# Performance work log

Measured on AMD Instinct MI355X. Metric: run time of the kernel, lower is better.

Reference implementation:

```python
import jax, jax.numpy as jnp
import numpy as np

B, T, C = 2, 2048, 2048
N_HEAD, N_KV_HEAD = 16, 4
HEAD_DIM = C // N_HEAD  # 128
N_REP = N_HEAD // N_KV_HEAD  # 4


def setup_inputs() -> dict:
    key = jax.random.key(0)
    ks = jax.random.split(key, 5)
    x = jax.random.normal(ks[0], (B, T, C), dtype=jnp.float32)
    # RoPE freqs (theta=10000), real cos/sin form of torch's complex freqs_cis
    inv_freq = 1.0 / (10000.0 ** (jnp.arange(0, HEAD_DIM, 2, dtype=jnp.float32) / HEAD_DIM))
    angles = jnp.arange(T, dtype=jnp.float32)[:, None] * inv_freq[None, :]  # [T, HEAD_DIM//2]
    freqs_cos = jnp.cos(angles)
    freqs_sin = jnp.sin(angles)
    s = 0.02
    wq = jax.random.normal(ks[1], (C, C), dtype=jnp.float32) * s
    wk = jax.random.normal(ks[2], (N_KV_HEAD * HEAD_DIM, C), dtype=jnp.float32) * s
    wv = jax.random.normal(ks[3], (N_KV_HEAD * HEAD_DIM, C), dtype=jnp.float32) * s
    wo = jax.random.normal(ks[4], (C, C), dtype=jnp.float32) * s
    return {"x": x, "freqs_cos": freqs_cos, "freqs_sin": freqs_sin,
            "wq": wq, "wk": wk, "wv": wv, "wo": wo}


def _apply_rotary(t, cos, sin):
    # t: [B, T, H, D]; pairs (even, odd) treated as complex, multiplied by cos+i*sin
    tr = t.reshape(*t.shape[:-1], -1, 2)  # [B,T,H,D/2,2]
    t0, t1 = tr[..., 0], tr[..., 1]
    c = cos[None, :, None, :]  # [1,T,1,D/2]
    s = sin[None, :, None, :]
    out = jnp.stack([t0 * c - t1 * s, t0 * s + t1 * c], axis=-1)
    return out.reshape(t.shape)


def reference(x, freqs_cos, freqs_sin, wq, wk, wv, wo):
    b, t, _ = x.shape
    xq = (x @ wq.T).reshape(b, t, N_HEAD, HEAD_DIM)
    xk = (x @ wk.T).reshape(b, t, N_KV_HEAD, HEAD_DIM)
    xv = (x @ wv.T).reshape(b, t, N_KV_HEAD, HEAD_DIM)
    xq = _apply_rotary(xq, freqs_cos, freqs_sin)
    xk = _apply_rotary(xk, freqs_cos, freqs_sin)
    # GQA: repeat_interleave kv heads to n_head
    xk_r = jnp.repeat(xk, N_REP, axis=2)
    xv_r = jnp.repeat(xv, N_REP, axis=2)
    # [B,H,T,D]
    q = xq.transpose(0, 2, 1, 3)
    k = xk_r.transpose(0, 2, 1, 3)
    v = xv_r.transpose(0, 2, 1, 3)
    scale = 1.0 / jnp.sqrt(jnp.float32(HEAD_DIM))
    scores = jnp.einsum('bhtd,bhsd->bhts', q, k) * scale
    causal = jnp.tril(jnp.ones((t, t), dtype=bool))
    scores = jnp.where(causal[None, None], scores, jnp.finfo(scores.dtype).min)
    attn = jax.nn.softmax(scores, axis=-1)
    y = jnp.einsum('bhts,bhsd->bhtd', attn, v)
    y = y.transpose(0, 2, 1, 3).reshape(b, t, C)
    return y @ wo.T
```

## Files before the change

kernel.cpp:

```cpp
#include <hip/hip_runtime.h>

typedef __attribute__((ext_vector_type(8))) __bf16 bf16x8;
typedef __attribute__((ext_vector_type(4))) __bf16 bf16x4;
typedef __attribute__((ext_vector_type(4))) float floatx4;

#define MFMA16x16x32 __builtin_amdgcn_mfma_f32_16x16x32_bf16

__device__ __forceinline__ void async_load16(const void* g, void* l) {
  __builtin_amdgcn_global_load_lds((const __attribute__((address_space(1))) void*)g,
                                   (__attribute__((address_space(3))) void*)l, 16, 0, 0);
}

__global__ __launch_bounds__(256) void cast_all_kernel(const float* __restrict__ x,
                                                       const float* __restrict__ wq,
                                                       const float* __restrict__ wk,
                                                       const float* __restrict__ wv,
                                                       const float* __restrict__ wo,
                                                       __bf16* __restrict__ dst) {
  int i = blockIdx.x * blockDim.x + threadIdx.x;
  const float* src;
  int off;
  if (i < 2097152)      { src = x;  off = 0; }
  else if (i < 3145728) { src = wq; off = 2097152; }
  else if (i < 3407872) { src = wk; off = 3145728; }
  else if (i < 3670016) { src = wv; off = 3407872; }
  else                  { src = wo; off = 3670016; }
  float4 v = ((const float4*)src)[i - off];
  bf16x4 o;
  o[0] = (__bf16)v.x; o[1] = (__bf16)v.y; o[2] = (__bf16)v.z; o[3] = (__bf16)v.w;
  *(bf16x4*)(dst + (size_t)i * 4) = o;
}

template <int MODE>
__global__ __launch_bounds__(256, 3) void gemm_bt(const __bf16* __restrict__ A,
                                                  const __bf16* __restrict__ Bw,
                                                  float* __restrict__ C,
                                                  const float* __restrict__ cs,
                                                  const float* __restrict__ sn,
                                                  __bf16* __restrict__ qb,
                                                  __bf16* __restrict__ kb,
                                                  __bf16* __restrict__ vtg,
                                                  int M, int N, int K) {
  __shared__ __bf16 As[128][64];
  __shared__ __bf16 Bs[128][64];
  const int tid = threadIdx.x;
  const int wave = tid >> 6, lane = tid & 63;
  const int quad = lane >> 4, l16 = lane & 15;
  const int wm = (wave >> 1) * 64, wn = (wave & 1) * 64;
  const int row0 = blockIdx.y * 128, col0 = blockIdx.x * 128;
  const int lr = lane >> 3, ls = lane & 7;
  const int segg = ls ^ lr;
  floatx4 acc[4][4] = {};
  const __bf16* Ab = A + (size_t)row0 * K + segg * 8;
  const __bf16* Bb = Bw + (size_t)col0 * K + segg * 8;
  for (int k0 = 0; k0 < K; k0 += 64) {
    __syncthreads();
#pragma unroll
    for (int i = 0; i < 4; i++) {
      int c = wave * 4 + i;
      int r = c * 8 + lr;
      async_load16(Ab + (size_t)r * K + k0, &As[c * 8][0]);
      async_load16(Bb + (size_t)r * K + k0, &Bs[c * 8][0]);
    }
    __syncthreads();
#pragma unroll
    for (int kk = 0; kk < 64; kk += 32) {
      bf16x8 af[4], bfr[4];
#pragma unroll
      for (int mt = 0; mt < 4; mt++) {
        int row = wm + mt * 16 + l16;
        int seg = ((kk >> 3) + quad) ^ (row & 7);
        af[mt] = *(const bf16x8*)&As[row][seg * 8];
      }
#pragma unroll
      for (int nt = 0; nt < 4; nt++) {
        int row = wn + nt * 16 + l16;
        int seg = ((kk >> 3) + quad) ^ (row & 7);
        bfr[nt] = *(const bf16x8*)&Bs[row][seg * 8];
      }
#pragma unroll
      for (int mt = 0; mt < 4; mt++)
#pragma unroll
        for (int nt = 0; nt < 4; nt++)
          acc[mt][nt] = MFMA16x16x32(af[mt], bfr[nt], acc[mt][nt], 0, 0, 0);
    }
  }
  if (MODE == 0) {
#pragma unroll
    for (int mt = 0; mt < 4; mt++)
#pragma unroll
      for (int nt = 0; nt < 4; nt++)
#pragma unroll
        for (int r = 0; r < 4; r++) {
          int row = row0 + wm + mt * 16 + quad * 4 + r;
          int col = col0 + wn + nt * 16 + l16;
          C[(size_t)row * N + col] = acc[mt][nt][r];
        }
  } else {
#pragma unroll
    for (int mt = 0; mt < 4; mt++)
#pragma unroll
      for (int nt = 0; nt < 4; nt++) {
        const int cbase = col0 + wn + nt * 16;
        const int c = cbase + l16;
#pragma unroll
        for (int r = 0; r < 4; r++) {
          int row = row0 + wm + mt * 16 + quad * 4 + r;
          int t = row & 2047;
          float v = acc[mt][nt][r];
          float vp = __shfl_xor(v, 1);
          if (cbase < 2048) {
            int i = (c & 127) >> 1;
            float co = cs[t * 64 + i], si = sn[t * 64 + i];
            qb[(size_t)row * 2048 + c] = (__bf16)(v * co + ((c & 1) ? vp : -vp) * si);
          } else if (cbase < 2560) {
            int i = (c & 127) >> 1;
            float co = cs[t * 64 + i], si = sn[t * 64 + i];
            kb[(size_t)row * 512 + c - 2048] = (__bf16)(v * co + ((c & 1) ? vp : -vp) * si);
          } else {
            int vd = c - 2560;
            vtg[((size_t)(row >> 11) * 512 + vd) * 2048 + t] = (__bf16)v;
          }
        }
      }
  }
}

__global__ __launch_bounds__(256, 2) void attn_kernel(const __bf16* __restrict__ qb,
                                                      const __bf16* __restrict__ kb,
                                                      const __bf16* __restrict__ vtg,
                                                      __bf16* __restrict__ yb) {
  const int id = blockIdx.x;
  const int q1 = id >> 8;
  const int cc = id & 255;
  const int kvh = cc & 3;
  const int b = (cc >> 2) & 1;
  const int s5 = (cc >> 3) & 31;
  const int tile = q1 ? (63 - s5) : s5;
  const int tid = threadIdx.x, wave = tid >> 6, lane = tid & 63;
  const int h = kvh * 4 + wave;
  const int quad = lane >> 4, l16 = lane & 15;
  const int q0 = tile * 32;
  __shared__ __bf16 Ks[2][64][128];
  __shared__ __bf16 Vt[2][128][64];
  __shared__ __bf16 Ps[4][2][16][64];
  const __bf16* kbase = kb + (size_t)b * 2048 * 512 + kvh * 128;
  const __bf16* vbase = vtg + ((size_t)b * 512 + kvh * 128) * 2048;
  const float cexp = 0.1275411391f;
  const int klr4 = lane >> 4, kls = lane & 15;
  const int vlr8 = lane >> 3, vls = lane & 7;

  auto stage = [&](int pb, int s0) {
#pragma unroll
    for (int i = 0; i < 4; i++) {
      int ch = wave * 4 + i;
      int row = ch * 4 + klr4;
      int sg = kls ^ (row & 7);
      async_load16(kbase + (size_t)(s0 + row) * 512 + sg * 8, &Ks[pb][ch * 4][0]);
    }
#pragma unroll
    for (int i = 0; i < 4; i++) {
      int ch = wave * 4 + i;
      int d = ch * 8 + vlr8;
      int sg = vls ^ (d & 7);
      async_load16(vbase + (size_t)d * 2048 + s0 + sg * 8, &Vt[pb][ch * 8][0]);
    }
  };

  bf16x8 qf[2][4];
#pragma unroll
  for (int mt = 0; mt < 2; mt++)
#pragma unroll
    for (int kc = 0; kc < 4; kc++)
      qf[mt][kc] = *(const bf16x8*)(qb + (size_t)(b * 2048 + q0 + mt * 16 + l16) * 2048 +
                                    h * 128 + kc * 32 + quad * 8);
  bf16x8 ones;
#pragma unroll
  for (int j = 0; j < 8; j++) ones[j] = (__bf16)1.0f;
  floatx4 o[2][8] = {};
  floatx4 lsum[2] = {};
  const int nblocks = (tile + 2) >> 1;

  stage(0, 0);
  __syncthreads();

  for (int it = 0; it < nblocks; it++) {
    const int cur = it & 1;
    const int s0 = it * 64;
    if (it + 1 < nblocks) stage(cur ^ 1, s0 + 64);
    floatx4 sacc[2][4] = {};
#pragma unroll
    for (int kc = 0; kc < 4; kc++) {
      bf16x8 bfr[4];
#pragma unroll
      for (int nt = 0; nt < 4; nt++) {
        int key = nt * 16 + l16;
        int seg = (kc * 4 + quad) ^ (key & 7);
        bfr[nt] = *(const bf16x8*)&Ks[cur][key][seg * 8];
      }
#pragma unroll
      for (int mt = 0; mt < 2; mt++)
#pragma unroll
        for (int nt = 0; nt < 4; nt++)
          sacc[mt][nt] = MFMA16x16x32(qf[mt][kc], bfr[nt], sacc[mt][nt], 0, 0, 0);
    }
    const bool diag = (it == nblocks - 1);
#pragma unroll
    for (int mt = 0; mt < 2; mt++)
#pragma unroll
      for (int r = 0; r < 4; r++) {
        const int row = quad * 4 + r;
        const int qg = q0 + mt * 16 + row;
#pragma unroll
        for (int nt = 0; nt < 4; nt++) {
          float p = __builtin_exp2f(sacc[mt][nt][r] * cexp);
          if (diag) { int keyg = s0 + nt * 16 + l16; p = (keyg <= qg) ? p : 0.f; }
          int col = nt * 16 + l16;
          Ps[wave][mt][row][(((col >> 3) ^ (row & 7)) << 3) + (col & 7)] = (__bf16)p;
        }
      }
#pragma unroll
    for (int c2 = 0; c2 < 2; c2++) {
      bf16x8 pa[2];
#pragma unroll
      for (int mt = 0; mt < 2; mt++) {
        int segp = ((c2 * 4 + quad) ^ (l16 & 7)) << 3;
        pa[mt] = *(const bf16x8*)&Ps[wave][mt][l16][segp];
        lsum[mt] = MFMA16x16x32(pa[mt], ones, lsum[mt], 0, 0, 0);
      }
#pragma unroll
      for (int dt = 0; dt < 8; dt++) {
        int row = dt * 16 + l16;
        int seg = (c2 * 4 + quad) ^ (row & 7);
        bf16x8 vf = *(const bf16x8*)&Vt[cur][row][seg * 8];
#pragma unroll
        for (int mt = 0; mt < 2; mt++)
          o[mt][dt] = MFMA16x16x32(pa[mt], vf, o[mt][dt], 0, 0, 0);
      }
    }
    __syncthreads();
  }
#pragma unroll
  for (int mt = 0; mt < 2; mt++) {
    float inv[4];
#pragma unroll
    for (int r = 0; r < 4; r++) inv[r] = 1.f / lsum[mt][r];
#pragma unroll
    for (int dt = 0; dt < 8; dt++)
#pragma unroll
      for (int r = 0; r < 4; r++) {
        int qg = q0 + mt * 16 + quad * 4 + r;
        yb[(size_t)(b * 2048 + qg) * 2048 + h * 128 + dt * 16 + l16] =
            (__bf16)(o[mt][dt][r] * inv[r]);
      }
  }
}

extern "C" void kernel_launch(void* const* d_in, const int* in_sizes, int n_in,
                              void* d_out, int out_size, void* d_ws, size_t ws_size,
                              hipStream_t stream) {
  const float* x  = (const float*)d_in[0];
  const float* fc = (const float*)d_in[1];
  const float* fs = (const float*)d_in[2];
  const float* wq = (const float*)d_in[3];
  const float* wk = (const float*)d_in[4];
  const float* wv = (const float*)d_in[5];
  const float* wo = (const float*)d_in[6];
  float* out = (float*)d_out;
  char* ws = (char*)d_ws;

  __bf16* xb   = (__bf16*)(ws);
  __bf16* wqkv = (__bf16*)(ws + 16777216);
  __bf16* wob  = (__bf16*)(ws + 29360128);
  __bf16* qbuf = (__bf16*)(ws + 37748736);
  __bf16* kbuf = (__bf16*)(ws + 54525952);
  __bf16* vtg  = (__bf16*)(ws + 58720256);
  __bf16* ybuf = (__bf16*)(ws + 62914560);

  cast_all_kernel<<<18432, 256, 0, stream>>>(x, wq, wk, wv, wo, xb);

  gemm_bt<1><<<dim3(24, 32), 256, 0, stream>>>(xb, wqkv, nullptr, fc, fs,
                                               qbuf, kbuf, vtg, 4096, 3072, 2048);

  attn_kernel<<<dim3(512), 256, 0, stream>>>(qbuf, kbuf, vtg, ybuf);

  gemm_bt<0><<<dim3(16, 32), 256, 0, stream>>>(ybuf, wob, out, nullptr, nullptr,
                                               nullptr, nullptr, nullptr, 4096, 2048, 2048);
}
```

Baseline: 309.4 us.

## Precompute LDS addresses, fold softmax scale into Q, add MFMA priority hints

```diff
diff --git a/kernel.cpp b/kernel.cpp
--- a/kernel.cpp
+++ b/kernel.cpp
@@ -112,7 +112,8 @@
           if (cbase < 2048) {
             int i = (c & 127) >> 1;
             float co = cs[t * 64 + i], si = sn[t * 64 + i];
-            qb[(size_t)row * 2048 + c] = (__bf16)(v * co + ((c & 1) ? vp : -vp) * si);
+            qb[(size_t)row * 2048 + c] =
+                (__bf16)((v * co + ((c & 1) ? vp : -vp) * si) * 0.1275411391f);
           } else if (cbase < 2560) {
             int i = (c & 127) >> 1;
             float co = cs[t * 64 + i], si = sn[t * 64 + i];
@@ -146,25 +147,50 @@
   __shared__ __bf16 Ps[4][2][16][64];
   const __bf16* kbase = kb + (size_t)b * 2048 * 512 + kvh * 128;
   const __bf16* vbase = vtg + ((size_t)b * 512 + kvh * 128) * 2048;
-  const float cexp = 0.1275411391f;
+
+  const int u16   = (quad ^ (l16 & 3)) * 16;
+  const int b2_64 = (l16 & 4) ? 64 : 0;
+  char* const ksb = (char*)Ks;
+  char* const vtb = (char*)Vt;
+  char* const psb = (char*)Ps + wave * 4096;
+  char* const kA0 = ksb + l16 * 256 + u16 + b2_64;
+  char* const kB0 = kA0 + 64 - 2 * b2_64;
+  char* const kA1 = kA0 + 16384;
+  char* const kB1 = kB0 + 16384;
+  char* const vA0 = vtb + l16 * 128 + u16 + b2_64;
+  char* const vB0 = vA0 + 64 - 2 * b2_64;
+  char* const vA1 = vA0 + 16384;
+  char* const vB1 = vB0 + 16384;
+  char* const prA = psb + l16 * 128 + u16 + b2_64;
+  char* const prB = prA + 64 - 2 * b2_64;
+  const int h16 = (l16 & 8) ? 16 : 0;
+  const int q64 = (quad & 1) * 64;
+  char* const pw00 = psb + quad * 512 + (l16 & 7) * 2 + h16 + q64;
+  char* const pw10 = psb + quad * 512 + (l16 & 7) * 2 + (16 - h16) + q64;
+  char* const pw01 = pw00 + 64 - 2 * q64;
+  char* const pw11 = pw10 + 64 - 2 * q64;
+
   const int klr4 = lane >> 4, kls = lane & 15;
   const int vlr8 = lane >> 3, vls = lane & 7;
+  const __bf16* ksrc[4];
+  const __bf16* vsrc[4];
+#pragma unroll
+  for (int i = 0; i < 4; i++) {
+    int row = (wave * 4 + i) * 4 + klr4;
+    ksrc[i] = kbase + (size_t)row * 512 + (kls ^ (row & 7)) * 8;
+    int d = (wave * 4 + i) * 8 + vlr8;
+    vsrc[i] = vbase + (size_t)d * 2048 + (vls ^ (d & 7)) * 8;
+  }
+  char* const kdst = ksb + wave * 4096;
+  char* const vdst = vtb + wave * 4096;
 
   auto stage = [&](int pb, int s0) {
 #pragma unroll
-    for (int i = 0; i < 4; i++) {
-      int ch = wave * 4 + i;
-      int row = ch * 4 + klr4;
-      int sg = kls ^ (row & 7);
-      async_load16(kbase + (size_t)(s0 + row) * 512 + sg * 8, &Ks[pb][ch * 4][0]);
-    }
-#pragma unroll
-    for (int i = 0; i < 4; i++) {
-      int ch = wave * 4 + i;
-      int d = ch * 8 + vlr8;
-      int sg = vls ^ (d & 7);
-      async_load16(vbase + (size_t)d * 2048 + s0 + sg * 8, &Vt[pb][ch * 8][0]);
-    }
+    for (int i = 0; i < 4; i++)
+      async_load16(ksrc[i] + (size_t)s0 * 512, kdst + pb * 16384 + i * 1024);
+#pragma unroll
+    for (int i = 0; i < 4; i++)
+      async_load16(vsrc[i] + s0, vdst + pb * 16384 + i * 1024);
   };
 
   bf16x8 qf[2][4];
@@ -188,56 +214,60 @@
     const int cur = it & 1;
     const int s0 = it * 64;
     if (it + 1 < nblocks) stage(cur ^ 1, s0 + 64);
+    const char* kA = cur ? kA1 : kA0;
+    const char* kB = cur ? kB1 : kB0;
+    const char* vA = cur ? vA1 : vA0;
+    const char* vB = cur ? vB1 : vB0;
     floatx4 sacc[2][4] = {};
+    __builtin_amdgcn_s_setprio(1);
 #pragma unroll
     for (int kc = 0; kc < 4; kc++) {
+      const char* kbp = (kc & 1) ? kB : kA;
       bf16x8 bfr[4];
 #pragma unroll
-      for (int nt = 0; nt < 4; nt++) {
-        int key = nt * 16 + l16;
-        int seg = (kc * 4 + quad) ^ (key & 7);
-        bfr[nt] = *(const bf16x8*)&Ks[cur][key][seg * 8];
-      }
+      for (int nt = 0; nt < 4; nt++)
+        bfr[nt] = *(const bf16x8*)(kbp + nt * 4096 + (kc >> 1) * 128);
 #pragma unroll
       for (int mt = 0; mt < 2; mt++)
 #pragma unroll
         for (int nt = 0; nt < 4; nt++)
           sacc[mt][nt] = MFMA16x16x32(qf[mt][kc], bfr[nt], sacc[mt][nt], 0, 0, 0);
     }
+    __builtin_amdgcn_s_setprio(0);
     const bool diag = (it == nblocks - 1);
 #pragma unroll
     for (int mt = 0; mt < 2; mt++)
 #pragma unroll
       for (int r = 0; r < 4; r++) {
-        const int row = quad * 4 + r;
-        const int qg = q0 + mt * 16 + row;
+        const int qg = q0 + mt * 16 + quad * 4 + r;
 #pragma unroll
         for (int nt = 0; nt < 4; nt++) {
-          float p = __builtin_exp2f(sacc[mt][nt][r] * cexp);
+          float p = __builtin_exp2f(sacc[mt][nt][r]);
           if (diag) { int keyg = s0 + nt * 16 + l16; p = (keyg <= qg) ? p : 0.f; }
-          int col = nt * 16 + l16;
-          Ps[wave][mt][row][(((col >> 3) ^ (row & 7)) << 3) + (col & 7)] = (__bf16)p;
+          char* w = (r & 1) ? ((nt < 2) ? pw10 : pw11) : ((nt < 2) ? pw00 : pw01);
+          *(__bf16*)(w + mt * 2048 + r * 128 + ((nt & 1) ^ (r >> 1)) * 32) = (__bf16)p;
         }
       }
+    __builtin_amdgcn_s_setprio(1);
 #pragma unroll
     for (int c2 = 0; c2 < 2; c2++) {
+      const char* pr = c2 ? prB : prA;
+      const char* vv = c2 ? vB : vA;
       bf16x8 pa[2];
 #pragma unroll
       for (int mt = 0; mt < 2; mt++) {
-        int segp = ((c2 * 4 + quad) ^ (l16 & 7)) << 3;
-        pa[mt] = *(const bf16x8*)&Ps[wave][mt][l16][segp];
+        pa[mt] = *(const bf16x8*)(pr + mt * 2048);
         lsum[mt] = MFMA16x16x32(pa[mt], ones, lsum[mt], 0, 0, 0);
       }
 #pragma unroll
       for (int dt = 0; dt < 8; dt++) {
-        int row = dt * 16 + l16;
-        int seg = (c2 * 4 + quad) ^ (row & 7);
-        bf16x8 vf = *(const bf16x8*)&Vt[cur][row][seg * 8];
+        bf16x8 vf = *(const bf16x8*)(vv + dt * 2048);
 #pragma unroll
         for (int mt = 0; mt < 2; mt++)
           o[mt][dt] = MFMA16x16x32(pa[mt], vf, o[mt][dt], 0, 0, 0);
       }
     }
+    __builtin_amdgcn_s_setprio(0);
     __syncthreads();
   }
 #pragma unroll
```

New measurement: 304.2 us. Within noise of the previous version (-1.7%).
